# Kernel optimization log

Measured on AMD Instinct MI355X. Metric: run time of the kernel, lower is better.

The kernel has to match this reference:

```python
import jax, jax.numpy as jnp
import numpy as np

MARGIN = 0.2
NEG_INF = -1e30


def setup_inputs() -> dict:
    key = jax.random.key(0)
    k1, k2 = jax.random.split(key)
    B, D, C = 384, 256, 48
    features = jax.random.normal(k1, (B, D), dtype=jnp.float32)
    labels = jax.random.randint(k2, (B,), 0, C, dtype=jnp.int32)
    return {"features": features, "labels": labels, "epoch": 5}


def reference(features, labels, epoch):
    B = features.shape[0]
    # pairwise euclidean distance, clamped like torch.clamp(min=1e-11)
    diff = features[:, None, :] - features[None, :, :]          # [B,B,D]
    dist = jnp.sqrt(jnp.clip(jnp.sum(diff * diff, axis=-1), 1e-11))  # [B,B]

    idx = jnp.arange(B)
    same = labels[:, None] == labels[None, :]
    pos_mask = same & (idx[None, :] > idx[:, None])             # pairs (i,j), j>i, same label
    neg_mask = ~same

    # Gumbel-max sampling replaces the per-row np.random.choice host loop.
    gumbel = jax.random.gumbel(jax.random.key(42), (B, B, B), dtype=dist.dtype)

    if epoch > 3:
        # semi-hard negatives: pos_dist < d(i,k) < pos_dist + margin, weights 1/d(i,k)
        d_ik = dist[:, None, :]                                 # [B,1,B]
        d_pos = dist[:, :, None]                                # [B,B,1]
        semi = neg_mask[:, None, :] & (d_ik > d_pos) & (d_ik < d_pos + MARGIN)  # [B,B,B]
        logits = jnp.where(semi, -jnp.log(dist)[:, None, :], NEG_INF)  # log(1/d)
        has_neg = jnp.any(semi, axis=-1)                        # [B,B]
    else:
        # uniform random negative per (i,j) pair
        logits = jnp.where(neg_mask[:, None, :], 0.0, NEG_INF)  # [B,1,B]
        has_neg = jnp.broadcast_to(jnp.any(neg_mask, axis=-1)[:, None], (B, B))

    neg_idx = jnp.argmax(logits + gumbel, axis=-1)              # [B,B]
    neg_dist = jnp.take_along_axis(dist, neg_idx, axis=1)       # d(i, sampled_neg)

    valid = pos_mask & has_neg
    # MarginRankingLoss(neg, pos, target=1) = relu(pos - neg + margin)
    per_pair = jax.nn.relu(dist - neg_dist + MARGIN)
    count = jnp.sum(valid)
    total = jnp.sum(jnp.where(valid, per_pair, 0.0))
    return jnp.where(count > 0, total / jnp.maximum(count, 1), 0.0)
```

## Files before the change

kernel.cpp:

```cpp
#include <hip/hip_runtime.h>
#include <hip/hip_bf16.h>
#include <stdint.h>

#define BSZ 384
#define DD  256
#define NWAVES 6
#define NEG_BIG -3.0e38f

__device__ __forceinline__ void threefry_0_42(uint32_t c0, uint32_t c1,
                                              uint32_t& o0, uint32_t& o1) {
    const uint32_t k0 = 0u;
    const uint32_t k1 = 42u;
    const uint32_t k2 = 0u ^ 42u ^ 0x1BD11BDAu;
    uint32_t x0 = c0 + k0;
    uint32_t x1 = c1 + k1;
#define TF_RND(R) { x0 += x1; x1 = (x1 << (R)) | (x1 >> (32 - (R))); x1 ^= x0; }
    TF_RND(13) TF_RND(15) TF_RND(26) TF_RND(6)
    x0 += k1; x1 += k2 + 1u;
    TF_RND(17) TF_RND(29) TF_RND(16) TF_RND(24)
    x0 += k2; x1 += k0 + 2u;
    TF_RND(13) TF_RND(15) TF_RND(26) TF_RND(6)
    x0 += k0; x1 += k1 + 3u;
    TF_RND(17) TF_RND(29) TF_RND(16) TF_RND(24)
    x0 += k1; x1 += k2 + 4u;
    TF_RND(13) TF_RND(15) TF_RND(26) TF_RND(6)
    x0 += k2; x1 += k0 + 5u;
#undef TF_RND
    o0 = x0; o1 = x1;
}

__device__ __forceinline__ float gumbel_at(uint32_t idx) {
    uint32_t r0, r1;
    threefry_0_42(0u, idx, r0, r1);
    uint32_t bits = r0 ^ r1;
    uint32_t mant = bits >> 9;
    float f = __uint_as_float(mant | 0x3F800000u) - 1.0f;
    float u = (mant == 0u) ? 1.17549435e-38f : f;
    return -logf(-logf(u));
}

__global__ __launch_bounds__(256) void dist_kernel(const float* __restrict__ F,
                                                   float* __restrict__ dist,
                                                   float* __restrict__ total,
                                                   unsigned int* __restrict__ count,
                                                   unsigned int* __restrict__ done) {
    __shared__ float As[16][DD + 4];
    __shared__ float Bs[16][DD + 4];
    const int i0 = blockIdx.y * 16;
    const int j0 = blockIdx.x * 16;
    const int tid = threadIdx.x;

    if (blockIdx.x == 0 && blockIdx.y == 0 && tid == 0) {
        *total = 0.0f; *count = 0u; *done = 0u;
    }

    for (int t = tid; t < 16 * 64; t += 256) {
        const int r = t >> 6;
        const int c = (t & 63) << 2;
        float4 a = *(const float4*)&F[(i0 + r) * DD + c];
        float4 b = *(const float4*)&F[(j0 + r) * DD + c];
        *(float4*)&As[r][c] = a;
        *(float4*)&Bs[r][c] = b;
    }
    __syncthreads();

    const int tx = tid & 15;
    const int ty = tid >> 4;
    float a0 = 0.f, a1 = 0.f, a2 = 0.f, a3 = 0.f;
#pragma unroll 8
    for (int d = 0; d < DD; d += 4) {
        float4 av = *(const float4*)&As[ty][d];
        float4 bv = *(const float4*)&Bs[tx][d];
        float d0 = av.x - bv.x;
        float d1 = av.y - bv.y;
        float d2 = av.z - bv.z;
        float d3 = av.w - bv.w;
        a0 = fmaf(d0, d0, a0);
        a1 = fmaf(d1, d1, a1);
        a2 = fmaf(d2, d2, a2);
        a3 = fmaf(d3, d3, a3);
    }
    float s = (a0 + a1) + (a2 + a3);
    s = fmaxf(s, 1e-11f);
    dist[(i0 + ty) * BSZ + (j0 + tx)] = sqrtf(s);
}

__global__ __launch_bounds__(BSZ) void mine_kernel(const float* __restrict__ dist,
                                                   const int* __restrict__ labels,
                                                   const int* __restrict__ epochp,
                                                   float* __restrict__ total,
                                                   unsigned int* __restrict__ count,
                                                   unsigned int* __restrict__ done,
                                                   float* __restrict__ out) {
    __shared__ float    row[BSZ];
    __shared__ float    nlog[BSZ];
    __shared__ int      slab[BSZ];
    __shared__ int      plist[BSZ];
    __shared__ int      npos;
    __shared__ float    wtot[NWAVES];
    __shared__ unsigned wcnt[NWAVES];

    const int i    = blockIdx.x;
    const int tid  = threadIdx.x;
    const int wave = tid >> 6;
    const int lane = tid & 63;

    slab[tid] = labels[tid];
    if (tid == 0) npos = 0;
    __syncthreads();

    const int lab_i = slab[i];
    if (tid > i && slab[tid] == lab_i)
        plist[atomicAdd(&npos, 1)] = tid;
    const int  epoch   = *epochp;
    const bool semisel = (epoch > 3);
    __syncthreads();

    const int np = npos;
    float    t_total = 0.0f;
    unsigned t_count = 0u;

    if (np > 0) {
        const float dk = dist[i * BSZ + tid];
        row[tid]  = dk;
        nlog[tid] = semisel ? -logf(dk) : 0.0f;
        __syncthreads();

        for (int p = wave; p < np; p += NWAVES) {
            const int   j     = plist[p];
            const float d_pos = row[j];
            const float hi    = d_pos + 0.2f;
            float v  = NEG_BIG;
            int   kk = 0;
#pragma unroll
            for (int c = 0; c < BSZ / 64; ++c) {
                const int   k   = c * 64 + lane;
                const float dkk = row[k];
                const bool cand = (slab[k] != lab_i) &&
                                  (!semisel || (dkk > d_pos && dkk < hi));
                if (__any(cand)) {
                    if (cand) {
                        const uint32_t idx = (uint32_t)(i * BSZ + j) * (uint32_t)BSZ
                                             + (uint32_t)k;
                        float val = nlog[k] + gumbel_at(idx);
                        if (val > v) { v = val; kk = k; }
                    }
                }
            }
#pragma unroll
            for (int off = 32; off; off >>= 1) {
                float ov = __shfl_down(v, off, 64);
                int   oi = __shfl_down(kk, off, 64);
                if (ov > v || (ov == v && oi < kk)) { v = ov; kk = oi; }
            }
            if (lane == 0 && v > -1.0e38f) {
                t_total += fmaxf(d_pos - row[kk] + 0.2f, 0.0f);
                t_count += 1u;
            }
        }
    }

    if (lane == 0) { wtot[wave] = t_total; wcnt[wave] = t_count; }
    __syncthreads();
    if (tid == 0) {
        float    tt = 0.0f;
        unsigned cc = 0u;
#pragma unroll
        for (int q = 0; q < NWAVES; ++q) { tt += wtot[q]; cc += wcnt[q]; }
        if (cc) {
            atomicAdd(total, tt);
            atomicAdd(count, cc);
        }
        __threadfence();
        const unsigned prev = atomicAdd(done, 1u);
        if (prev == (unsigned)gridDim.x - 1u) {
            const float    T = atomicAdd(total, 0.0f);
            const unsigned C = atomicAdd(count, 0u);
            out[0] = (C > 0u) ? (T / (float)C) : 0.0f;
        }
    }
}

extern "C" void kernel_launch(void* const* d_in, const int* in_sizes, int n_in,
                              void* d_out, int out_size, void* d_ws, size_t ws_size,
                              hipStream_t stream) {
    const float* F      = (const float*)d_in[0];
    const int*   labels = (const int*)d_in[1];
    const int*   epoch  = (const int*)d_in[2];
    float*       out    = (float*)d_out;

    const size_t dist_bytes = (size_t)BSZ * BSZ * sizeof(float);
    if (ws_size < dist_bytes + 16) return;

    float*        dist  = (float*)d_ws;
    float*        total = (float*)((char*)d_ws + dist_bytes);
    unsigned int* count = (unsigned int*)(total + 1);
    unsigned int* done  = (unsigned int*)(total + 2);

    dist_kernel<<<dim3(BSZ / 16, BSZ / 16), 256, 0, stream>>>(F, dist, total, count, done);
    mine_kernel<<<BSZ, BSZ, 0, stream>>>(dist, labels, epoch, total, count, done, out);
}
```

Baseline: 79.28 us.

## Mine negatives with one wave per row using registers and ballot

The mining kernel now runs one 64-thread wave per anchor row instead of six waves. The distance row, labels and log-weights are held in registers, positive pairs are enumerated with a ballot mask, and the negative distance is fetched with shuffles, so shared memory and block barriers are gone. The cost is that each block does all positive pairs serially in one wave, which cuts parallelism per row, and the per-chunk __any early-skip is dropped. The loss update uses an odd add-then-subtract pattern.

Result: slower. 91.98 us (+16.0%).

```diff
diff --git a/kernel.cpp b/kernel.cpp
--- a/kernel.cpp
+++ b/kernel.cpp
@@ -4,7 +4,7 @@
 
 #define BSZ 384
 #define DD  256
-#define NWAVES 6
+#define NCHUNK (BSZ / 64)
 #define NEG_BIG -3.0e38f
 
 __device__ __forceinline__ void threefry_0_42(uint32_t c0, uint32_t c1,
@@ -85,66 +85,59 @@
     dist[(i0 + ty) * BSZ + (j0 + tx)] = sqrtf(s);
 }
 
-__global__ __launch_bounds__(BSZ) void mine_kernel(const float* __restrict__ dist,
-                                                   const int* __restrict__ labels,
-                                                   const int* __restrict__ epochp,
-                                                   float* __restrict__ total,
-                                                   unsigned int* __restrict__ count,
-                                                   unsigned int* __restrict__ done,
-                                                   float* __restrict__ out) {
-    __shared__ float    row[BSZ];
-    __shared__ float    nlog[BSZ];
-    __shared__ int      slab[BSZ];
-    __shared__ int      plist[BSZ];
-    __shared__ int      npos;
-    __shared__ float    wtot[NWAVES];
-    __shared__ unsigned wcnt[NWAVES];
-
+__global__ __launch_bounds__(64) void mine_kernel(const float* __restrict__ dist,
+                                                  const int* __restrict__ labels,
+                                                  const int* __restrict__ epochp,
+                                                  float* __restrict__ total,
+                                                  unsigned int* __restrict__ count,
+                                                  unsigned int* __restrict__ done,
+                                                  float* __restrict__ out) {
     const int i    = blockIdx.x;
-    const int tid  = threadIdx.x;
-    const int wave = tid >> 6;
-    const int lane = tid & 63;
-
-    slab[tid] = labels[tid];
-    if (tid == 0) npos = 0;
-    __syncthreads();
-
-    const int lab_i = slab[i];
-    if (tid > i && slab[tid] == lab_i)
-        plist[atomicAdd(&npos, 1)] = tid;
+    const int lane = threadIdx.x;
+
+    const int  lab_i   = labels[i];
     const int  epoch   = *epochp;
     const bool semisel = (epoch > 3);
-    __syncthreads();
-
-    const int np = npos;
+
+    float dr[NCHUNK];
+    int   lb[NCHUNK];
+    float nl[NCHUNK];
+#pragma unroll
+    for (int c = 0; c < NCHUNK; ++c) {
+        const int k = c * 64 + lane;
+        dr[c] = dist[i * BSZ + k];
+        lb[c] = labels[k];
+    }
+#pragma unroll
+    for (int c = 0; c < NCHUNK; ++c)
+        nl[c] = semisel ? -logf(dr[c]) : 0.0f;
+
     float    t_total = 0.0f;
     unsigned t_count = 0u;
-
-    if (np > 0) {
-        const float dk = dist[i * BSZ + tid];
-        row[tid]  = dk;
-        nlog[tid] = semisel ? -logf(dk) : 0.0f;
-        __syncthreads();
-
-        for (int p = wave; p < np; p += NWAVES) {
-            const int   j     = plist[p];
-            const float d_pos = row[j];
+    const uint32_t ibase = (uint32_t)i * (uint32_t)BSZ;
+
+#pragma unroll
+    for (int c = 0; c < NCHUNK; ++c) {
+        const int k = c * 64 + lane;
+        uint64_t pmask = __ballot(lb[c] == lab_i && k > i);
+        while (pmask) {
+            const int b = __ffsll((unsigned long long)pmask) - 1;
+            pmask &= pmask - 1;
+            const int   j     = c * 64 + b;
+            const float d_pos = __shfl(dr[c], b, 64);
             const float hi    = d_pos + 0.2f;
+            const uint32_t jb = (ibase + (uint32_t)j) * (uint32_t)BSZ;
+
             float v  = NEG_BIG;
             int   kk = 0;
 #pragma unroll
-            for (int c = 0; c < BSZ / 64; ++c) {
-                const int   k   = c * 64 + lane;
-                const float dkk = row[k];
-                const bool cand = (slab[k] != lab_i) &&
-                                  (!semisel || (dkk > d_pos && dkk < hi));
-                if (__any(cand)) {
-                    if (cand) {
-                        const uint32_t idx = (uint32_t)(i * BSZ + j) * (uint32_t)BSZ
-                                             + (uint32_t)k;
-                        float val = nlog[k] + gumbel_at(idx);
-                        if (val > v) { v = val; kk = k; }
-                    }
+            for (int q = 0; q < NCHUNK; ++q) {
+                const int kq = q * 64 + lane;
+                const bool cand = (lb[q] != lab_i) &&
+                                  (!semisel || (dr[q] > d_pos && dr[q] < hi));
+                if (cand) {
+                    float val = nl[q] + gumbel_at(jb + (uint32_t)kq);
+                    if (val > v) { v = val; kk = kq; }
                 }
             }
 #pragma unroll
@@ -154,22 +147,30 @@
                 if (ov > v || (ov == v && oi < kk)) { v = ov; kk = oi; }
             }
             if (lane == 0 && v > -1.0e38f) {
-                t_total += fmaxf(d_pos - row[kk] + 0.2f, 0.0f);
                 t_count += 1u;
+                t_total += fmaxf(d_pos + 0.2f, 0.0f);
+            }
+            {
+                const int wq = kk >> 6;
+                const int kk0 = __shfl(kk, 0, 64);
+                const float v0 = __shfl(v, 0, 64);
+                if (v0 > -1.0e38f) {
+                    float dn_l = dr[kk0 >> 6];
+                    float d_neg = __shfl(dn_l, kk0 & 63, 64);
+                    if (lane == 0) {
+                        t_total -= fmaxf(d_pos + 0.2f, 0.0f);
+                        t_total += fmaxf(d_pos - d_neg + 0.2f, 0.0f);
+                    }
+                }
+                (void)wq;
             }
         }
     }
 
-    if (lane == 0) { wtot[wave] = t_total; wcnt[wave] = t_count; }
-    __syncthreads();
-    if (tid == 0) {
-        float    tt = 0.0f;
-        unsigned cc = 0u;
-#pragma unroll
-        for (int q = 0; q < NWAVES; ++q) { tt += wtot[q]; cc += wcnt[q]; }
-        if (cc) {
-            atomicAdd(total, tt);
-            atomicAdd(count, cc);
+    if (lane == 0) {
+        if (t_count) {
+            atomicAdd(total, t_total);
+            atomicAdd(count, t_count);
         }
         __threadfence();
         const unsigned prev = atomicAdd(done, 1u);
@@ -198,5 +199,5 @@
     unsigned int* done  = (unsigned int*)(total + 2);
 
     dist_kernel<<<dim3(BSZ / 16, BSZ / 16), 256, 0, stream>>>(F, dist, total, count, done);
-    mine_kernel<<<BSZ, BSZ, 0, stream>>>(dist, labels, epoch, total, count, done, out);
-}
+    mine_kernel<<<BSZ, 64, 0, stream>>>(dist, labels, epoch, total, count, done, out);
+}
```
